# Performance work log

Hardware: AMD Instinct MI355X
Metric: run time of the kernel (lower is better)

Reference implementation:

```python
import jax, jax.numpy as jnp
import numpy as np

M, B, S, D, H = 8, 4, 512, 512, 8
HD = D // H  # head_dim = 64


def setup_inputs() -> dict:
    key = jax.random.key(0)
    k1, k2, k3 = jax.random.split(key, 3)
    x = jax.random.normal(k1, (M, B, S, D), dtype=jnp.float32)
    qkv_weight = jax.random.normal(k2, (M, D, 3 * D), dtype=jnp.float32) * 0.02
    proj_weight = jax.random.normal(k3, (M, D, D), dtype=jnp.float32) * 0.02
    return {"x": x, "qkv_weight": qkv_weight, "proj_weight": proj_weight}


def reference(x, qkv_weight, proj_weight):
    m, b, s, d = x.shape
    # model-axis batched QKV projection
    qkv = jnp.einsum('mbti,mio->mbto', x, qkv_weight)
    q, k, v = jnp.split(qkv, 3, axis=-1)
    # [m, b, h, s, hd]
    q = q.reshape(m, b, s, H, HD).transpose(0, 1, 3, 2, 4)
    k = k.reshape(m, b, s, H, HD).transpose(0, 1, 3, 2, 4)
    v = v.reshape(m, b, s, H, HD).transpose(0, 1, 3, 2, 4)
    att = jnp.einsum('mbhqd,mbhkd->mbhqk', q, k) / jnp.sqrt(jnp.float32(HD))
    causal = jnp.tril(jnp.ones((s, s), dtype=bool))
    att = jnp.where(causal, att, jnp.float32(-jnp.inf))
    att = jax.nn.softmax(att, axis=-1)
    y = jnp.einsum('mbhqk,mbhkd->mbhqd', att, v)
    y = y.transpose(0, 1, 3, 2, 4).reshape(m, b, s, d)
    return jnp.einsum('mbti,mio->mbto', y, proj_weight)
```

## Files before the change

### kernel.cpp

```cpp
#include <hip/hip_runtime.h>
#include <hip/hip_bf16.h>


typedef unsigned short u16;
typedef unsigned int u32;
typedef __attribute__((ext_vector_type(8))) short short8;
typedef __attribute__((ext_vector_type(4))) float f32x4;
typedef __attribute__((ext_vector_type(4))) unsigned short u16x4;
typedef __attribute__((ext_vector_type(8))) unsigned short u16x8;
typedef __attribute__((ext_vector_type(2))) unsigned int u32x2;

#define MFMA16(a, b, c) __builtin_amdgcn_mfma_f32_16x16x32_bf16((a), (b), (c), 0, 0, 0)

__device__ __forceinline__ u16 f2bf(float f) {
  union { __hip_bfloat16 h; u16 u; } cv;
  cv.h = __float2bfloat16(f);
  return cv.u;
}

__global__ __launch_bounds__(256) void wtrans_kernel(const float* __restrict__ in,
                                                     u16* __restrict__ out, int R, int C) {
  __shared__ float t[32][33];
  int m = blockIdx.z;
  const float* pin = in + (size_t)m * R * C;
  u16* pout = out + (size_t)m * R * C;
  int c0 = blockIdx.x * 32, r0 = blockIdx.y * 32;
  int tx = threadIdx.x, ty = threadIdx.y;
#pragma unroll
  for (int i = 0; i < 4; ++i) {
    int r = ty + i * 8;
    t[r][tx] = pin[(size_t)(r0 + r) * C + c0 + tx];
  }
  __syncthreads();
#pragma unroll
  for (int i = 0; i < 4; ++i) {
    int r = ty + i * 8;
    pout[(size_t)(c0 + r) * R + r0 + tx] = f2bf(t[tx][r]);
  }
}

__global__ __launch_bounds__(256) void qkv_gemm_kernel(const float* __restrict__ X,
                                                       const u16* __restrict__ WT,
                                                       u16* __restrict__ Q,
                                                       u16* __restrict__ K,
                                                       u16* __restrict__ VT) {
  __shared__ u16 As[128][40];
  __shared__ u16 Bs[128][40];
  int m = blockIdx.z;
  const float* A = X + (size_t)m * 2048 * 512;
  const u16* BT = WT + (size_t)m * 1536 * 512;
  int r0 = blockIdx.y * 128, c0 = blockIdx.x * 128;
  int t = threadIdx.x;
  int lane = t & 63, w = t >> 6;
  int wr = (w >> 1) * 64, wc = (w & 1) * 64;
  int fr = lane & 15, fc = lane >> 4;

  f32x4 acc[4][4];
#pragma unroll
  for (int i = 0; i < 4; ++i)
#pragma unroll
    for (int j = 0; j < 4; ++j) acc[i][j] = f32x4{0.f, 0.f, 0.f, 0.f};

  for (int kk = 0; kk < 512; kk += 32) {
#pragma unroll
    for (int i = 0; i < 4; ++i) {
      int idx = t + i * 256;
      int row = idx >> 3, f4 = idx & 7;
      f32x4 v = *(const f32x4*)(A + (size_t)(r0 + row) * 512 + kk + f4 * 4);
      u16x4 pk = {f2bf(v[0]), f2bf(v[1]), f2bf(v[2]), f2bf(v[3])};
      *(u16x4*)&As[row][f4 * 4] = pk;
    }
#pragma unroll
    for (int i = 0; i < 2; ++i) {
      int u = t + i * 256;
      int col = u >> 2, kc = u & 3;
      u16x8 v = *(const u16x8*)(BT + (size_t)(c0 + col) * 512 + kk + kc * 8);
      *(u16x8*)&Bs[col][kc * 8] = v;
    }
    __syncthreads();
    short8 af[4], bf[4];
#pragma unroll
    for (int i = 0; i < 4; ++i) af[i] = *(const short8*)&As[wr + i * 16 + fr][fc * 8];
#pragma unroll
    for (int j = 0; j < 4; ++j) bf[j] = *(const short8*)&Bs[wc + j * 16 + fr][fc * 8];
#pragma unroll
    for (int i = 0; i < 4; ++i)
#pragma unroll
      for (int j = 0; j < 4; ++j) acc[i][j] = MFMA16(af[i], bf[j], acc[i][j]);
    __syncthreads();
  }

  int seg = c0 >> 9;
#pragma unroll
  for (int i = 0; i < 4; ++i) {
#pragma unroll
    for (int j = 0; j < 4; ++j) {
#pragma unroll
      for (int r = 0; r < 4; ++r) {
        int grow = r0 + wr + i * 16 + fc * 4 + r;
        int gcol = c0 + wc + j * 16 + fr;
        int b = grow >> 9, s = grow & 511;
        int cc = gcol & 511;
        int hh = cc >> 6, hd = cc & 63;
        size_t headoff = (size_t)((m * 4 + b) * 8 + hh) * 32768;
        u16 val = f2bf(acc[i][j][r]);
        if (seg == 0)      Q[headoff + s * 64 + hd] = val;
        else if (seg == 1) K[headoff + s * 64 + hd] = val;
        else               VT[headoff + hd * 512 + s] = val;
      }
    }
  }
}

__global__ __launch_bounds__(256) void attn_kernel(const u16* __restrict__ Qg,
                                                   const u16* __restrict__ Kg,
                                                   const u16* __restrict__ VTg,
                                                   u16* __restrict__ Yg) {
  __shared__ u16 Ks[2][64][72];
  __shared__ u16 Vs[2][64][72];
  __shared__ u16 Pl[4][16][72];
  int bid = blockIdx.x;
  int qt = bid >> 8;
  int g = bid & 255;
  int h = g & 7, mb = g >> 3;
  int t = threadIdx.x, lane = t & 63, w = t >> 6;
  int fr = lane & 15, fc = lane >> 4;
  size_t hoff = ((size_t)mb * 8 + h) * 32768;
  const u16* Q = Qg + hoff;
  const u16* K = Kg + hoff;
  const u16* V = VTg + hoff;
  int qrow = qt * 64 + w * 16 + fr;
  const float SC = 0.125f * 1.44269504088896340736f;

  short8 qf0 = *(const short8*)(Q + (size_t)qrow * 64 + fc * 8);
  short8 qf1 = *(const short8*)(Q + (size_t)qrow * 64 + 32 + fc * 8);

  f32x4 acc[4];
#pragma unroll
  for (int d = 0; d < 4; ++d) acc[d] = f32x4{0.f, 0.f, 0.f, 0.f};
  float mst = -1e30f, lst = 0.f;

  int u0 = 2 * t, u1 = 2 * t + 1;
  int kr0 = u0 >> 3, kc0 = (u0 & 7) * 8;
  int kr1 = u1 >> 3, kc1 = (u1 & 7) * 8;

  {
    u16x8 a0 = *(const u16x8*)(K + (size_t)kr0 * 64 + kc0);
    u16x8 a1 = *(const u16x8*)(K + (size_t)kr1 * 64 + kc1);
    u16x8 b0 = *(const u16x8*)(V + (size_t)kr0 * 512 + kc0);
    u16x8 b1 = *(const u16x8*)(V + (size_t)kr1 * 512 + kc1);
    *(u16x8*)&Ks[0][kr0][kc0] = a0;
    *(u16x8*)&Ks[0][kr1][kc1] = a1;
    *(u16x8*)&Vs[0][kr0][kc0] = b0;
    *(u16x8*)&Vs[0][kr1][kc1] = b1;
  }
  __syncthreads();

  for (int kt = 0; kt <= qt; ++kt) {
    int cur = kt & 1;
    bool pref = kt < qt;
    u16x8 nk0, nk1, nv0, nv1;
    if (pref) {
      int kbn = (kt + 1) * 64;
      nk0 = *(const u16x8*)(K + (size_t)(kbn + kr0) * 64 + kc0);
      nk1 = *(const u16x8*)(K + (size_t)(kbn + kr1) * 64 + kc1);
      nv0 = *(const u16x8*)(V + (size_t)kr0 * 512 + kbn + kc0);
      nv1 = *(const u16x8*)(V + (size_t)kr1 * 512 + kbn + kc1);
    }

    f32x4 st[4];
#pragma unroll
    for (int sub = 0; sub < 4; ++sub) {
      short8 kf0 = *(const short8*)&Ks[cur][sub * 16 + fr][fc * 8];
      short8 kf1 = *(const short8*)&Ks[cur][sub * 16 + fr][32 + fc * 8];
      f32x4 z = f32x4{0.f, 0.f, 0.f, 0.f};
      z = MFMA16(kf0, qf0, z);
      st[sub] = MFMA16(kf1, qf1, z);
    }

    float p[4][4];
    float mt = -3e30f;
    bool diag = (kt == qt);
    int qloc = w * 16 + fr;
#pragma unroll
    for (int sub = 0; sub < 4; ++sub)
#pragma unroll
      for (int r = 0; r < 4; ++r) {
        float v = st[sub][r] * SC;
        if (diag && (sub * 16 + fc * 4 + r) > qloc) v = -1e30f;
        p[sub][r] = v;
        mt = fmaxf(mt, v);
      }
    mt = fmaxf(mt, __shfl_xor(mt, 16));
    mt = fmaxf(mt, __shfl_xor(mt, 32));
    float mn = fmaxf(mst, mt);
    float al = __builtin_amdgcn_exp2f(mst - mn);
    mst = mn;
    float rs = 0.f;
#pragma unroll
    for (int sub = 0; sub < 4; ++sub)
#pragma unroll
      for (int r = 0; r < 4; ++r) {
        float e = __builtin_amdgcn_exp2f(p[sub][r] - mn);
        p[sub][r] = e;
        rs += e;
      }
    rs += __shfl_xor(rs, 16);
    rs += __shfl_xor(rs, 32);
    lst = lst * al + rs;
#pragma unroll
    for (int d = 0; d < 4; ++d) acc[d] *= al;

#pragma unroll
    for (int sub = 0; sub < 4; ++sub) {
      u32 lo = (u32)f2bf(p[sub][0]) | ((u32)f2bf(p[sub][1]) << 16);
      u32 hi = (u32)f2bf(p[sub][2]) | ((u32)f2bf(p[sub][3]) << 16);
      *(u32x2*)&Pl[w][fr][sub * 16 + fc * 4] = u32x2{lo, hi};
    }

#pragma unroll
    for (int dt = 0; dt < 4; ++dt)
#pragma unroll
      for (int kc = 0; kc < 2; ++kc) {
        short8 vf = *(const short8*)&Vs[cur][dt * 16 + fr][kc * 32 + fc * 8];
        short8 pb = *(const short8*)&Pl[w][fr][kc * 32 + fc * 8];
        acc[dt] = MFMA16(vf, pb, acc[dt]);
      }

    if (pref) {
      *(u16x8*)&Ks[cur ^ 1][kr0][kc0] = nk0;
      *(u16x8*)&Ks[cur ^ 1][kr1][kc1] = nk1;
      *(u16x8*)&Vs[cur ^ 1][kr0][kc0] = nv0;
      *(u16x8*)&Vs[cur ^ 1][kr1][kc1] = nv1;
    }
    __syncthreads();
  }

  float inv = 1.0f / lst;
#pragma unroll
  for (int dt = 0; dt < 4; ++dt) {
    u16x4 o = {f2bf(acc[dt][0] * inv), f2bf(acc[dt][1] * inv),
               f2bf(acc[dt][2] * inv), f2bf(acc[dt][3] * inv)};
    *(u16x4*)(Yg + ((size_t)mb * 512 + qrow) * 512 + h * 64 + dt * 16 + fc * 4) = o;
  }
}

__global__ __launch_bounds__(256) void proj_gemm_kernel(const u16* __restrict__ Y,
                                                        const u16* __restrict__ PT,
                                                        float* __restrict__ OUT) {
  __shared__ u16 As[128][40];
  __shared__ u16 Bs[128][40];
  int m = blockIdx.z;
  const u16* A = Y + (size_t)m * 2048 * 512;
  const u16* BT = PT + (size_t)m * 512 * 512;
  float* C = OUT + (size_t)m * 2048 * 512;
  int r0 = blockIdx.y * 128, c0 = blockIdx.x * 128;
  int t = threadIdx.x;
  int lane = t & 63, w = t >> 6;
  int wr = (w >> 1) * 64, wc = (w & 1) * 64;
  int fr = lane & 15, fc = lane >> 4;

  f32x4 acc[4][4];
#pragma unroll
  for (int i = 0; i < 4; ++i)
#pragma unroll
    for (int j = 0; j < 4; ++j) acc[i][j] = f32x4{0.f, 0.f, 0.f, 0.f};

  for (int kk = 0; kk < 512; kk += 32) {
#pragma unroll
    for (int i = 0; i < 2; ++i) {
      int u = t + i * 256;
      int row = u >> 2, kc = u & 3;
      u16x8 v = *(const u16x8*)(A + (size_t)(r0 + row) * 512 + kk + kc * 8);
      *(u16x8*)&As[row][kc * 8] = v;
    }
#pragma unroll
    for (int i = 0; i < 2; ++i) {
      int u = t + i * 256;
      int col = u >> 2, kc = u & 3;
      u16x8 v = *(const u16x8*)(BT + (size_t)(c0 + col) * 512 + kk + kc * 8);
      *(u16x8*)&Bs[col][kc * 8] = v;
    }
    __syncthreads();
    short8 af[4], bf[4];
#pragma unroll
    for (int i = 0; i < 4; ++i) af[i] = *(const short8*)&As[wr + i * 16 + fr][fc * 8];
#pragma unroll
    for (int j = 0; j < 4; ++j) bf[j] = *(const short8*)&Bs[wc + j * 16 + fr][fc * 8];
#pragma unroll
    for (int i = 0; i < 4; ++i)
#pragma unroll
      for (int j = 0; j < 4; ++j) acc[i][j] = MFMA16(af[i], bf[j], acc[i][j]);
    __syncthreads();
  }
#pragma unroll
  for (int i = 0; i < 4; ++i)
#pragma unroll
    for (int j = 0; j < 4; ++j)
#pragma unroll
      for (int r = 0; r < 4; ++r) {
        int grow = r0 + wr + i * 16 + fc * 4 + r;
        int gcol = c0 + wc + j * 16 + fr;
        C[(size_t)grow * 512 + gcol] = acc[i][j][r];
      }
}

extern "C" void kernel_launch(void* const* d_in, const int* in_sizes, int n_in,
                              void* d_out, int out_size, void* d_ws, size_t ws_size,
                              hipStream_t stream) {
  const float* x = (const float*)d_in[0];
  const float* wqkv = (const float*)d_in[1];
  const float* wproj = (const float*)d_in[2];
  float* out = (float*)d_out;

  u16* p = (u16*)d_ws;
  u16* wqkvT = p;  p += (size_t)8 * 1536 * 512;
  u16* wprojT = p; p += (size_t)8 * 512 * 512;
  u16* qb = p;     p += (size_t)8388608;
  u16* kb = p;     p += (size_t)8388608;
  u16* vtb = p;    p += (size_t)8388608;
  u16* yb = p;     p += (size_t)8388608;

  wtrans_kernel<<<dim3(48, 16, 8), dim3(32, 8), 0, stream>>>(wqkv, wqkvT, 512, 1536);
  wtrans_kernel<<<dim3(16, 16, 8), dim3(32, 8), 0, stream>>>(wproj, wprojT, 512, 512);
  qkv_gemm_kernel<<<dim3(12, 16, 8), 256, 0, stream>>>(x, wqkvT, qb, kb, vtb);
  attn_kernel<<<2048, 256, 0, stream>>>(qb, kb, vtb, yb);
  proj_gemm_kernel<<<dim3(4, 16, 8), 256, 0, stream>>>(yb, wprojT, out);
}
```

Measured before the change: 225.9 us.

## Pre-cast X to bf16 and load GEMM tiles via global_load_lds

Adds a separate kernel that casts the fp32 input to bf16 into a workspace buffer, shared with the attention output buffer. Both GEMMs then fill their LDS tiles with direct global-to-LDS 16-byte loads into unpadded 32-wide rows instead of going through registers. The aim is to cut VGPR traffic and conversion work inside the GEMM loops. In exchange it adds a full extra read and write pass over X, and the unpadded LDS layout may cause bank conflicts on the fragment reads.

```diff
diff --git a/kernel.cpp b/kernel.cpp
--- a/kernel.cpp
+++ b/kernel.cpp
@@ -16,6 +16,24 @@
   union { __hip_bfloat16 h; u16 u; } cv;
   cv.h = __float2bfloat16(f);
   return cv.u;
+}
+
+__device__ __forceinline__ void gl_lds16(const u16* g, u16* l) {
+  __builtin_amdgcn_global_load_lds(
+      (const __attribute__((address_space(1))) void*)g,
+      (__attribute__((address_space(3))) void*)l, 16, 0, 0);
+}
+
+__global__ __launch_bounds__(256) void xcast_kernel(const float* __restrict__ in,
+                                                    u16* __restrict__ out, long n8) {
+  long stride = (long)gridDim.x * 256;
+  for (long i = blockIdx.x * 256L + threadIdx.x; i < n8; i += stride) {
+    f32x4 a = *(const f32x4*)(in + i * 8);
+    f32x4 b = *(const f32x4*)(in + i * 8 + 4);
+    u16x8 o = {f2bf(a[0]), f2bf(a[1]), f2bf(a[2]), f2bf(a[3]),
+               f2bf(b[0]), f2bf(b[1]), f2bf(b[2]), f2bf(b[3])};
+    *(u16x8*)(out + i * 8) = o;
+  }
 }
 
 __global__ __launch_bounds__(256) void wtrans_kernel(const float* __restrict__ in,
@@ -39,15 +57,15 @@
   }
 }
 
-__global__ __launch_bounds__(256) void qkv_gemm_kernel(const float* __restrict__ X,
+__global__ __launch_bounds__(256) void qkv_gemm_kernel(const u16* __restrict__ XB,
                                                        const u16* __restrict__ WT,
                                                        u16* __restrict__ Q,
                                                        u16* __restrict__ K,
                                                        u16* __restrict__ VT) {
-  __shared__ u16 As[128][40];
-  __shared__ u16 Bs[128][40];
+  __shared__ __attribute__((aligned(16))) u16 As[128 * 32];
+  __shared__ __attribute__((aligned(16))) u16 Bs[128 * 32];
   int m = blockIdx.z;
-  const float* A = X + (size_t)m * 2048 * 512;
+  const u16* A = XB + (size_t)m * 2048 * 512;
   const u16* BT = WT + (size_t)m * 1536 * 512;
   int r0 = blockIdx.y * 128, c0 = blockIdx.x * 128;
   int t = threadIdx.x;
@@ -55,6 +73,15 @@
   int wr = (w >> 1) * 64, wc = (w & 1) * 64;
   int fr = lane & 15, fc = lane >> 4;
 
+  int u0 = w * 128 + lane;
+  int u1 = w * 128 + 64 + lane;
+  int ar0 = u0 >> 2, ak0 = (u0 & 3) * 8;
+  int ar1 = u1 >> 2, ak1 = (u1 & 3) * 8;
+  u16* lbase0 = &As[0] + (size_t)(w * 128) * 8;
+  u16* lbase1 = &As[0] + (size_t)(w * 128 + 64) * 8;
+  u16* lbb0 = &Bs[0] + (size_t)(w * 128) * 8;
+  u16* lbb1 = &Bs[0] + (size_t)(w * 128 + 64) * 8;
+
   f32x4 acc[4][4];
 #pragma unroll
   for (int i = 0; i < 4; ++i)
@@ -62,27 +89,16 @@
     for (int j = 0; j < 4; ++j) acc[i][j] = f32x4{0.f, 0.f, 0.f, 0.f};
 
   for (int kk = 0; kk < 512; kk += 32) {
-#pragma unroll
-    for (int i = 0; i < 4; ++i) {
-      int idx = t + i * 256;
-      int row = idx >> 3, f4 = idx & 7;
-      f32x4 v = *(const f32x4*)(A + (size_t)(r0 + row) * 512 + kk + f4 * 4);
-      u16x4 pk = {f2bf(v[0]), f2bf(v[1]), f2bf(v[2]), f2bf(v[3])};
-      *(u16x4*)&As[row][f4 * 4] = pk;
-    }
-#pragma unroll
-    for (int i = 0; i < 2; ++i) {
-      int u = t + i * 256;
-      int col = u >> 2, kc = u & 3;
-      u16x8 v = *(const u16x8*)(BT + (size_t)(c0 + col) * 512 + kk + kc * 8);
-      *(u16x8*)&Bs[col][kc * 8] = v;
-    }
+    gl_lds16(A + (size_t)(r0 + ar0) * 512 + kk + ak0, lbase0);
+    gl_lds16(A + (size_t)(r0 + ar1) * 512 + kk + ak1, lbase1);
+    gl_lds16(BT + (size_t)(c0 + ar0) * 512 + kk + ak0, lbb0);
+    gl_lds16(BT + (size_t)(c0 + ar1) * 512 + kk + ak1, lbb1);
     __syncthreads();
     short8 af[4], bf[4];
 #pragma unroll
-    for (int i = 0; i < 4; ++i) af[i] = *(const short8*)&As[wr + i * 16 + fr][fc * 8];
-#pragma unroll
-    for (int j = 0; j < 4; ++j) bf[j] = *(const short8*)&Bs[wc + j * 16 + fr][fc * 8];
+    for (int i = 0; i < 4; ++i) af[i] = *(const short8*)&As[(wr + i * 16 + fr) * 32 + fc * 8];
+#pragma unroll
+    for (int j = 0; j < 4; ++j) bf[j] = *(const short8*)&Bs[(wc + j * 16 + fr) * 32 + fc * 8];
 #pragma unroll
     for (int i = 0; i < 4; ++i)
 #pragma unroll
@@ -248,8 +264,8 @@
 __global__ __launch_bounds__(256) void proj_gemm_kernel(const u16* __restrict__ Y,
                                                         const u16* __restrict__ PT,
                                                         float* __restrict__ OUT) {
-  __shared__ u16 As[128][40];
-  __shared__ u16 Bs[128][40];
+  __shared__ __attribute__((aligned(16))) u16 As[128 * 32];
+  __shared__ __attribute__((aligned(16))) u16 Bs[128 * 32];
   int m = blockIdx.z;
   const u16* A = Y + (size_t)m * 2048 * 512;
   const u16* BT = PT + (size_t)m * 512 * 512;
@@ -260,6 +276,15 @@
   int wr = (w >> 1) * 64, wc = (w & 1) * 64;
   int fr = lane & 15, fc = lane >> 4;
 
+  int u0 = w * 128 + lane;
+  int u1 = w * 128 + 64 + lane;
+  int ar0 = u0 >> 2, ak0 = (u0 & 3) * 8;
+  int ar1 = u1 >> 2, ak1 = (u1 & 3) * 8;
+  u16* lbase0 = &As[0] + (size_t)(w * 128) * 8;
+  u16* lbase1 = &As[0] + (size_t)(w * 128 + 64) * 8;
+  u16* lbb0 = &Bs[0] + (size_t)(w * 128) * 8;
+  u16* lbb1 = &Bs[0] + (size_t)(w * 128 + 64) * 8;
+
   f32x4 acc[4][4];
 #pragma unroll
   for (int i = 0; i < 4; ++i)
@@ -267,26 +292,16 @@
     for (int j = 0; j < 4; ++j) acc[i][j] = f32x4{0.f, 0.f, 0.f, 0.f};
 
   for (int kk = 0; kk < 512; kk += 32) {
-#pragma unroll
-    for (int i = 0; i < 2; ++i) {
-      int u = t + i * 256;
-      int row = u >> 2, kc = u & 3;
-      u16x8 v = *(const u16x8*)(A + (size_t)(r0 + row) * 512 + kk + kc * 8);
-      *(u16x8*)&As[row][kc * 8] = v;
-    }
-#pragma unroll
-    for (int i = 0; i < 2; ++i) {
-      int u = t + i * 256;
-      int col = u >> 2, kc = u & 3;
-      u16x8 v = *(const u16x8*)(BT + (size_t)(c0 + col) * 512 + kk + kc * 8);
-      *(u16x8*)&Bs[col][kc * 8] = v;
-    }
+    gl_lds16(A + (size_t)(r0 + ar0) * 512 + kk + ak0, lbase0);
+    gl_lds16(A + (size_t)(r0 + ar1) * 512 + kk + ak1, lbase1);
+    gl_lds16(BT + (size_t)(c0 + ar0) * 512 + kk + ak0, lbb0);
+    gl_lds16(BT + (size_t)(c0 + ar1) * 512 + kk + ak1, lbb1);
     __syncthreads();
     short8 af[4], bf[4];
 #pragma unroll
-    for (int i = 0; i < 4; ++i) af[i] = *(const short8*)&As[wr + i * 16 + fr][fc * 8];
-#pragma unroll
-    for (int j = 0; j < 4; ++j) bf[j] = *(const short8*)&Bs[wc + j * 16 + fr][fc * 8];
+    for (int i = 0; i < 4; ++i) af[i] = *(const short8*)&As[(wr + i * 16 + fr) * 32 + fc * 8];
+#pragma unroll
+    for (int j = 0; j < 4; ++j) bf[j] = *(const short8*)&Bs[(wc + j * 16 + fr) * 32 + fc * 8];
 #pragma unroll
     for (int i = 0; i < 4; ++i)
 #pragma unroll
@@ -319,11 +334,12 @@
   u16* qb = p;     p += (size_t)8388608;
   u16* kb = p;     p += (size_t)8388608;
   u16* vtb = p;    p += (size_t)8388608;
-  u16* yb = p;     p += (size_t)8388608;
-
+  u16* xyb = p;    p += (size_t)8388608;
+
+  xcast_kernel<<<2048, 256, 0, stream>>>(x, xyb, (long)8 * 4 * 512 * 512 / 8);
   wtrans_kernel<<<dim3(48, 16, 8), dim3(32, 8), 0, stream>>>(wqkv, wqkvT, 512, 1536);
   wtrans_kernel<<<dim3(16, 16, 8), dim3(32, 8), 0, stream>>>(wproj, wprojT, 512, 512);
-  qkv_gemm_kernel<<<dim3(12, 16, 8), 256, 0, stream>>>(x, wqkvT, qb, kb, vtb);
-  attn_kernel<<<2048, 256, 0, stream>>>(qb, kb, vtb, yb);
-  proj_gemm_kernel<<<dim3(4, 16, 8), 256, 0, stream>>>(yb, wprojT, out);
-}
+  qkv_gemm_kernel<<<dim3(12, 16, 8), 256, 0, stream>>>(xyb, wqkvT, qb, kb, vtb);
+  attn_kernel<<<2048, 256, 0, stream>>>(qb, kb, vtb, xyb);
+  proj_gemm_kernel<<<dim3(4, 16, 8), 256, 0, stream>>>(xyb, wprojT, out);
+}
```

New measurement: 220.7 us. 1.02x faster.
